# Kernel optimization log

Hardware: AMD Instinct MI355X
Metric: run time of the kernel (lower is better)

Reference implementation:

```python
import jax, jax.numpy as jnp
import numpy as np

NUM_HEADS = 8
NUM_GROUPS = 8
EPS = 1e-5


def group_norm(x, gamma, beta):
    # x: [B, C, H, W], 8 groups over channel dim
    B, C, H, W = x.shape
    xg = x.reshape(B, NUM_GROUPS, C // NUM_GROUPS, H, W)
    mean = xg.mean(axis=(2, 3, 4), keepdims=True)
    var = xg.var(axis=(2, 3, 4), keepdims=True)
    xn = ((xg - mean) * jax.lax.rsqrt(var + EPS)).reshape(B, C, H, W)
    return xn * gamma[None, :, None, None] + beta[None, :, None, None]


def conv1x1(x, w, b):
    # w: [O, C] (1x1 conv kernel squeezed), x: [B, C, H, W]
    return jnp.einsum('oc,bchw->bohw', w, x) + b[None, :, None, None]


def setup_inputs() -> dict:
    key = jax.random.key(0)
    ks = jax.random.split(key, 6)
    B, C, H, W = 16, 512, 32, 32
    x = jax.random.normal(ks[0], (B, C, H, W), dtype=jnp.float32)
    norm_w = jnp.ones((C,), jnp.float32)
    norm_b = jnp.zeros((C,), jnp.float32)
    s = 1.0 / np.sqrt(C)
    qkv_w = jax.random.uniform(ks[1], (3 * C, C), jnp.float32, -s, s)
    qkv_b = jax.random.uniform(ks[2], (3 * C,), jnp.float32, -s, s)
    proj_w = jax.random.uniform(ks[3], (C, C), jnp.float32, -s, s)
    proj_b = jax.random.uniform(ks[4], (C,), jnp.float32, -s, s)
    return {"x": x, "norm_w": norm_w, "norm_b": norm_b,
            "qkv_w": qkv_w, "qkv_b": qkv_b, "proj_w": proj_w, "proj_b": proj_b}


def reference(x, norm_w, norm_b, qkv_w, qkv_b, proj_w, proj_b):
    B, C, H, W = x.shape
    hd = C // NUM_HEADS  # head dim
    h = group_norm(x, norm_w, norm_b)
    qkv = conv1x1(h, qkv_w, qkv_b)                 # [B, 3C, H, W]
    q, k, v = jnp.split(qkv, 3, axis=1)
    q = q.reshape(B, NUM_HEADS, hd, H * W)
    k = k.reshape(B, NUM_HEADS, hd, H * W)
    v = v.reshape(B, NUM_HEADS, hd, H * W)
    scale = hd ** (-0.5)
    attn = jax.nn.softmax(jnp.einsum('bhci,bhcj->bhij', q, k) * scale, axis=-1)
    h = jnp.einsum('bhij,bhcj->bhci', attn, v).reshape(B, C, H, W)
    h = conv1x1(h, proj_w, proj_b)
    return x + h
```

## Files before the change

kernel.cpp:

```cpp
#include <hip/hip_runtime.h>
#include <hip/hip_bf16.h>


typedef __bf16 bf16;
typedef __attribute__((ext_vector_type(8))) __bf16 bf16x8;
typedef __attribute__((ext_vector_type(4))) float f32x4;
typedef __attribute__((ext_vector_type(16))) float f32x16;
typedef __attribute__((ext_vector_type(4))) unsigned int u32x4;

#define SCALE_Q 0.18033688f

__device__ __forceinline__ bf16x8 ld8(const bf16* p) {
    return *reinterpret_cast<const bf16x8*>(p);
}

__device__ __forceinline__ void gl_lds16(const void* g, void* l) {
    __builtin_amdgcn_global_load_lds(
        (const __attribute__((address_space(1))) void*)g,
        (__attribute__((address_space(3))) void*)l, 16, 0, 0);
}

__global__ __launch_bounds__(256) void cvt_fp32_bf16(const float* __restrict__ src,
                                                     bf16* __restrict__ dst, int n) {
    int i = (blockIdx.x * blockDim.x + threadIdx.x) * 4;
    int stride = gridDim.x * blockDim.x * 4;
    for (; i < n; i += stride) {
        float4 f = *reinterpret_cast<const float4*>(src + i);
        dst[i + 0] = (bf16)f.x;
        dst[i + 1] = (bf16)f.y;
        dst[i + 2] = (bf16)f.z;
        dst[i + 3] = (bf16)f.w;
    }
}

__global__ __launch_bounds__(256) void gn_stats(const float* __restrict__ x,
                                                float2* __restrict__ stats) {
    int bg = blockIdx.x;
    const float* base = x + (size_t)bg * 65536;
    float s = 0.f, sq = 0.f;
    for (int i = threadIdx.x * 4; i < 65536; i += 256 * 4) {
        float4 f = *reinterpret_cast<const float4*>(base + i);
        s += f.x + f.y + f.z + f.w;
        sq += f.x * f.x + f.y * f.y + f.z * f.z + f.w * f.w;
    }
    #pragma unroll
    for (int off = 32; off > 0; off >>= 1) {
        s += __shfl_down(s, off);
        sq += __shfl_down(sq, off);
    }
    __shared__ float ls[4], lq[4];
    int wave = threadIdx.x >> 6, lane = threadIdx.x & 63;
    if (lane == 0) { ls[wave] = s; lq[wave] = sq; }
    __syncthreads();
    if (threadIdx.x == 0) {
        s = ls[0] + ls[1] + ls[2] + ls[3];
        sq = lq[0] + lq[1] + lq[2] + lq[3];
        float mean = s * (1.f / 65536.f);
        float var = sq * (1.f / 65536.f) - mean * mean;
        stats[bg] = make_float2(mean, rsqrtf(var + 1e-5f));
    }
}

__global__ __launch_bounds__(256) void gn_apply_t(const float* __restrict__ x,
                                                  const float* __restrict__ gamma,
                                                  const float* __restrict__ beta,
                                                  const float2* __restrict__ stats,
                                                  bf16* __restrict__ hnT) {
    int b = blockIdx.z, ct = blockIdx.y, pt = blockIdx.x;
    __shared__ float tile[64][65];
    int t = threadIdx.x;
    const float* xb = x + ((size_t)b * 512 + ct * 64) * 1024 + pt * 64;
    #pragma unroll
    for (int r = 0; r < 16; r++) {
        int cl = r * 4 + (t >> 6);
        int pl = t & 63;
        tile[cl][pl] = xb[(size_t)cl * 1024 + pl];
    }
    __syncthreads();
    float2 mr = stats[b * 8 + ct];
    int cl = t & 63;
    float g = gamma[ct * 64 + cl], be = beta[ct * 64 + cl];
    bf16* ob = hnT + ((size_t)b * 1024 + pt * 64) * 512 + ct * 64;
    #pragma unroll
    for (int r = 0; r < 16; r++) {
        int pl = r * 4 + (t >> 6);
        float v = (tile[cl][pl] - mr.x) * mr.y * g + be;
        ob[(size_t)pl * 512 + cl] = (bf16)v;
    }
}

__device__ __forceinline__ void gemm_stage(const bf16* __restrict__ A,
                                           const bf16* __restrict__ B,
                                           char* smem, int buf,
                                           int m_blk, int n_blk, int k0,
                                           int wave, int lane) {
    char* Al = smem + buf * 32768;
    char* Bl = Al + 16384;
    #pragma unroll
    for (int i = 0; i < 4; i++) {
        int seg = i * 4 + wave;
        int r = seg * 8 + (lane >> 3);
        int cg = (lane & 7) ^ (r & 7);
        gl_lds16((const char*)(A + (size_t)(m_blk + r) * 512 + k0) + cg * 16,
                 Al + seg * 1024);
        gl_lds16((const char*)(B + (size_t)(n_blk + r) * 512 + k0) + cg * 16,
                 Bl + seg * 1024);
    }
}

__device__ __forceinline__ void gemm_compute(const char* smem, int buf,
                                             int wave, int lane,
                                             f32x4 (&acc)[4][4]) {
    const char* Al = smem + buf * 32768;
    const char* Bl = Al + 16384;
    int l15 = lane & 15, hi = lane >> 4;
    int mb = (wave >> 1) * 64, nb = (wave & 1) * 64;
    #pragma unroll
    for (int kc = 0; kc < 2; kc++) {
        int ck = kc * 4 + hi;
        bf16x8 a[4], b[4];
        #pragma unroll
        for (int mf = 0; mf < 4; mf++) {
            int row = mb + mf * 16 + l15;
            a[mf] = *reinterpret_cast<const bf16x8*>(Al + row * 128 + (ck ^ (row & 7)) * 16);
        }
        #pragma unroll
        for (int nf = 0; nf < 4; nf++) {
            int row = nb + nf * 16 + l15;
            b[nf] = *reinterpret_cast<const bf16x8*>(Bl + row * 128 + (ck ^ (row & 7)) * 16);
        }
        #pragma unroll
        for (int mf = 0; mf < 4; mf++)
            #pragma unroll
            for (int nf = 0; nf < 4; nf++)
                acc[mf][nf] = __builtin_amdgcn_mfma_f32_16x16x32_bf16(
                    a[mf], b[nf], acc[mf][nf], 0, 0, 0);
    }
}

#define GEMM_LDS_LOOP(A_, B_)                                   \
    __shared__ char smem[65536];                                \
    f32x4 acc[4][4] = {};                                       \
    {                                                           \
        gemm_stage(A_, B_, smem, 0, m_blk, n_blk, 0, wave, lane); \
        __syncthreads();                                        \
        int buf = 0;                                            \
        for (int ks = 0; ks < 8; ks++) {                        \
            if (ks < 7)                                         \
                gemm_stage(A_, B_, smem, buf ^ 1, m_blk, n_blk, (ks + 1) * 64, wave, lane); \
            gemm_compute(smem, buf, wave, lane, acc);           \
            __syncthreads();                                    \
            buf ^= 1;                                           \
        }                                                       \
    }

__global__ __launch_bounds__(256, 2) void gemm_qk(const bf16* __restrict__ hnT,
                                                  const bf16* __restrict__ wqkv,
                                                  const float* __restrict__ qkv_b,
                                                  bf16* __restrict__ qk_t) {
    int b = blockIdx.z;
    int wave = threadIdx.x >> 6, lane = threadIdx.x & 63;
    int m_blk = blockIdx.x * 128;
    int n_blk = blockIdx.y * 128;
    const bf16* A = hnT + (size_t)b * 1024 * 512;
    GEMM_LDS_LOOP(A, wqkv)
    bf16* out = qk_t + (size_t)b * 1024 * 1024;
    int l15 = lane & 15;
    int col0 = n_blk + (wave & 1) * 64 + l15;
    int row0 = m_blk + (wave >> 1) * 64 + (lane >> 4) * 4;
    #pragma unroll
    for (int nf = 0; nf < 4; nf++) {
        int col = col0 + nf * 16;
        float bias = qkv_b[col];
        float scl = (col < 512) ? SCALE_Q : 1.0f;
        #pragma unroll
        for (int mf = 0; mf < 4; mf++)
            #pragma unroll
            for (int r = 0; r < 4; r++)
                out[(size_t)(row0 + mf * 16 + r) * 1024 + col] =
                    (bf16)((acc[mf][nf][r] + bias) * scl);
    }
}

__global__ __launch_bounds__(256, 2) void gemm_v(const bf16* __restrict__ wv,
                                                 const bf16* __restrict__ hnT,
                                                 const float* __restrict__ qkv_b,
                                                 bf16* __restrict__ vbuf) {
    int b = blockIdx.z;
    int wave = threadIdx.x >> 6, lane = threadIdx.x & 63;
    int m_blk = blockIdx.x * 128;
    int n_blk = blockIdx.y * 128;
    const bf16* Bm = hnT + (size_t)b * 1024 * 512;
    GEMM_LDS_LOOP(wv, Bm)
    bf16* out = vbuf + (size_t)b * 512 * 1024;
    int l15 = lane & 15;
    int col0 = n_blk + (wave & 1) * 64 + l15;
    int row0 = m_blk + (wave >> 1) * 64 + (lane >> 4) * 4;
    #pragma unroll
    for (int mf = 0; mf < 4; mf++)
        #pragma unroll
        for (int r = 0; r < 4; r++) {
            int row = row0 + mf * 16 + r;
            float bias = qkv_b[1024 + row];
            #pragma unroll
            for (int nf = 0; nf < 4; nf++)
                out[(size_t)row * 1024 + col0 + nf * 16] = (bf16)(acc[mf][nf][r] + bias);
        }
}

__global__ __launch_bounds__(256, 2) void gemm_proj(const bf16* __restrict__ wproj,
                                                    const bf16* __restrict__ attnT,
                                                    const float* __restrict__ proj_b,
                                                    const float* __restrict__ x,
                                                    float* __restrict__ out) {
    int b = blockIdx.z;
    int wave = threadIdx.x >> 6, lane = threadIdx.x & 63;
    int m_blk = blockIdx.x * 128;
    int n_blk = blockIdx.y * 128;
    const bf16* Bm = attnT + (size_t)b * 1024 * 512;
    GEMM_LDS_LOOP(wproj, Bm)
    const float* xb = x + (size_t)b * 512 * 1024;
    float* ob = out + (size_t)b * 512 * 1024;
    int l15 = lane & 15;
    int col0 = n_blk + (wave & 1) * 64 + l15;
    int row0 = m_blk + (wave >> 1) * 64 + (lane >> 4) * 4;
    #pragma unroll
    for (int mf = 0; mf < 4; mf++)
        #pragma unroll
        for (int r = 0; r < 4; r++) {
            int row = row0 + mf * 16 + r;
            float bias = proj_b[row];
            #pragma unroll
            for (int nf = 0; nf < 4; nf++) {
                size_t idx = (size_t)row * 1024 + col0 + nf * 16;
                ob[idx] = acc[mf][nf][r] + bias + xb[idx];
            }
        }
}

__global__ __launch_bounds__(256, 4) void attn_kernel(const bf16* __restrict__ qk_t,
                                                      const bf16* __restrict__ vbuf,
                                                      bf16* __restrict__ attnT) {
    int flat = blockIdx.x;
    int it = flat >> 7;
    int bh = flat & 127;
    int b = bh >> 3, h = bh & 7;
    int wave = threadIdx.x >> 6, lane = threadIdx.x & 63;
    int l31 = lane & 31, hi = lane >> 5;
    int i0 = it * 128 + wave * 32;
    const bf16* qkb = qk_t + (size_t)b * 1024 * 1024;
    const bf16* kbase = qkb + 512 + h * 64;
    const bf16* vb = vbuf + ((size_t)b * 512 + h * 64) * 1024;

    __shared__ __align__(16) char smem[32768];

    bf16x8 bq[4];
    #pragma unroll
    for (int kc = 0; kc < 4; kc++)
        bq[kc] = ld8(qkb + (size_t)(i0 + l31) * 1024 + h * 64 + kc * 16 + hi * 8);

    f32x16 oacc[2] = {};
    float l_part = 0.f;

#define ATTN_STAGE(bufi, j0_)                                                        \
    {                                                                                \
        char* Kl = smem + (bufi) * 16384;                                            \
        char* Vl = Kl + 8192;                                                        \
        _Pragma("unroll")                                                            \
        for (int i = 0; i < 2; i++) {                                                \
            int seg = wave + i * 4;                                                  \
            int r = seg * 8 + (lane >> 3);                                           \
            int cg = (lane & 7) ^ (r & 7);                                           \
            gl_lds16((const char*)(kbase + (size_t)((j0_) + r) * 1024) + cg * 16,    \
                     Kl + seg * 1024);                                               \
            gl_lds16((const char*)(vb + (size_t)r * 1024 + (j0_)) + cg * 16,         \
                     Vl + seg * 1024);                                               \
        }                                                                            \
    }

    ATTN_STAGE(0, 0)
    __syncthreads();
    int buf = 0;

    for (int t = 0; t < 16; t++) {
        if (t < 15) ATTN_STAGE(buf ^ 1, (t + 1) * 64)

        const char* Kl = smem + buf * 16384;
        const char* Vl = Kl + 8192;
        int rx = l31 & 7;

        bf16x8 kf[2][4];
        #pragma unroll
        for (int jb = 0; jb < 2; jb++)
            #pragma unroll
            for (int kc = 0; kc < 4; kc++)
                kf[jb][kc] = *reinterpret_cast<const bf16x8*>(
                    Kl + (jb * 32 + l31) * 128 + (((kc & 1) * 2 + hi + (kc >> 1) * 4) ^ rx) * 16);

        f32x16 s[2] = {};
        #pragma unroll
        for (int kc = 0; kc < 4; kc++) {
            s[0] = __builtin_amdgcn_mfma_f32_32x32x16_bf16(kf[0][kc], bq[kc], s[0], 0, 0, 0);
            s[1] = __builtin_amdgcn_mfma_f32_32x32x16_bf16(kf[1][kc], bq[kc], s[1], 0, 0, 0);
        }

        bf16x8 vf[2][4];
        #pragma unroll
        for (int df = 0; df < 2; df++)
            #pragma unroll
            for (int ks = 0; ks < 4; ks++)
                vf[df][ks] = *reinterpret_cast<const bf16x8*>(
                    Vl + (df * 32 + l31) * 128 + ((ks * 2 + hi) ^ rx) * 16);

        unsigned int pk0[2][4], pk1[2][4];
        #pragma unroll
        for (int jb = 0; jb < 2; jb++)
            #pragma unroll
            for (int m = 0; m < 4; m++) {
                float e0 = exp2f(s[jb][m * 4 + 0]);
                float e1 = exp2f(s[jb][m * 4 + 1]);
                float e2 = exp2f(s[jb][m * 4 + 2]);
                float e3 = exp2f(s[jb][m * 4 + 3]);
                l_part += (e0 + e1) + (e2 + e3);
                asm("v_cvt_pk_bf16_f32 %0, %1, %2" : "=v"(pk0[jb][m]) : "v"(e0), "v"(e1));
                asm("v_cvt_pk_bf16_f32 %0, %1, %2" : "=v"(pk1[jb][m]) : "v"(e2), "v"(e3));
            }

        bf16x8 af[4];
        #pragma unroll
        for (int jb = 0; jb < 2; jb++)
            #pragma unroll
            for (int tt = 0; tt < 2; tt++) {
                unsigned int a0 = pk0[jb][tt * 2], b0 = pk0[jb][tt * 2 + 1];
                unsigned int a1 = pk1[jb][tt * 2], b1 = pk1[jb][tt * 2 + 1];
                asm("v_permlane32_swap_b32 %0, %1" : "+v"(a0), "+v"(b0));
                asm("v_permlane32_swap_b32 %0, %1" : "+v"(a1), "+v"(b1));
                u32x4 w = {a0, a1, b0, b1};
                af[jb * 2 + tt] = __builtin_bit_cast(bf16x8, w);
            }

        #pragma unroll
        for (int ks = 0; ks < 4; ks++) {
            oacc[0] = __builtin_amdgcn_mfma_f32_32x32x16_bf16(af[ks], vf[0][ks], oacc[0], 0, 0, 0);
            oacc[1] = __builtin_amdgcn_mfma_f32_32x32x16_bf16(af[ks], vf[1][ks], oacc[1], 0, 0, 0);
        }

        __syncthreads();
        buf ^= 1;
    }
#undef ATTN_STAGE

    float lsum = l_part + __shfl_xor(l_part, 32);
    float inv = 1.f / lsum;

    bf16* O_l = (bf16*)smem;
    #pragma unroll
    for (int reg = 0; reg < 16; reg++) {
        int qrow = (reg & 3) + 8 * (reg >> 2) + 4 * hi;
        float iv = __shfl(inv, qrow);
        O_l[(wave * 32 + qrow) * 72 + l31]      = (bf16)(oacc[0][reg] * iv);
        O_l[(wave * 32 + qrow) * 72 + 32 + l31] = (bf16)(oacc[1][reg] * iv);
    }
    __syncthreads();
    {
        int tt = threadIdx.x;
        int il = tt >> 1, half = tt & 1;
        const bf16* lsrc = O_l + il * 72 + half * 32;
        bf16* gdst = attnT + ((size_t)b * 1024 + it * 128 + il) * 512 + h * 64 + half * 32;
        #pragma unroll
        for (int k = 0; k < 4; k++)
            *reinterpret_cast<bf16x8*>(gdst + k * 8) =
                *reinterpret_cast<const bf16x8*>(lsrc + k * 8);
    }
}

extern "C" void kernel_launch(void* const* d_in, const int* in_sizes, int n_in,
                              void* d_out, int out_size, void* d_ws, size_t ws_size,
                              hipStream_t stream) {
    (void)in_sizes; (void)n_in; (void)out_size; (void)ws_size;
    const float* x      = (const float*)d_in[0];
    const float* norm_w = (const float*)d_in[1];
    const float* norm_b = (const float*)d_in[2];
    const float* qkv_w  = (const float*)d_in[3];
    const float* qkv_b  = (const float*)d_in[4];
    const float* proj_w = (const float*)d_in[5];
    const float* proj_b = (const float*)d_in[6];
    float* out = (float*)d_out;

    char* w = (char*)d_ws;
    bf16* wqkv  = (bf16*)w;
    bf16* wproj = wqkv + (size_t)1536 * 512;
    float2* stats = (float2*)(wproj + (size_t)512 * 512);
    bf16* hnT   = (bf16*)((char*)stats + 1024);
    bf16* qk_t  = hnT + (size_t)16 * 1024 * 512;
    bf16* vbuf  = qk_t + (size_t)16 * 1024 * 1024;
    bf16* attnT = vbuf + (size_t)16 * 512 * 1024;

    cvt_fp32_bf16<<<768, 256, 0, stream>>>(qkv_w, wqkv, 1536 * 512);
    cvt_fp32_bf16<<<256, 256, 0, stream>>>(proj_w, wproj, 512 * 512);
    gn_stats<<<128, 256, 0, stream>>>(x, stats);
    gn_apply_t<<<dim3(16, 8, 16), 256, 0, stream>>>(x, norm_w, norm_b, stats, hnT);
    gemm_qk<<<dim3(8, 8, 16), 256, 0, stream>>>(hnT, wqkv, qkv_b, qk_t);
    gemm_v<<<dim3(4, 8, 16), 256, 0, stream>>>(wqkv + (size_t)1024 * 512, hnT, qkv_b, vbuf);
    attn_kernel<<<1024, 256, 0, stream>>>(qk_t, vbuf, attnT);
    gemm_proj<<<dim3(4, 8, 16), 256, 0, stream>>>(wproj, attnT, proj_b, x, out);
}
```

Measured before the change: 147.8 us.

## Fuse weight casts, groupnorm passes and QKV GEMMs; relax attention pipeline barriers

Merges the two weight-conversion kernels into one launch. Fuses the groupnorm stats and apply-transpose into one kernel with one block per (batch, group). Merges the Q/K and V GEMMs into a single launch split by blockIdx.y. The attention loop now uses raw s_barrier with explicit vmcnt waits instead of __syncthreads, so the next tile's loads can overlap compute, and the K-fragment LDS index pattern is changed. Fewer launches and less sync are the goal; the risks are that 128 groupnorm blocks underuse the GPU and that the new K indexing may not match the Q fragment order.

```diff
diff --git a/kernel.cpp b/kernel.cpp
--- a/kernel.cpp
+++ b/kernel.cpp
@@ -20,25 +20,31 @@
         (__attribute__((address_space(3))) void*)l, 16, 0, 0);
 }
 
-__global__ __launch_bounds__(256) void cvt_fp32_bf16(const float* __restrict__ src,
-                                                     bf16* __restrict__ dst, int n) {
-    int i = (blockIdx.x * blockDim.x + threadIdx.x) * 4;
-    int stride = gridDim.x * blockDim.x * 4;
-    for (; i < n; i += stride) {
-        float4 f = *reinterpret_cast<const float4*>(src + i);
-        dst[i + 0] = (bf16)f.x;
-        dst[i + 1] = (bf16)f.y;
-        dst[i + 2] = (bf16)f.z;
-        dst[i + 3] = (bf16)f.w;
-    }
-}
-
-__global__ __launch_bounds__(256) void gn_stats(const float* __restrict__ x,
-                                                float2* __restrict__ stats) {
+__global__ __launch_bounds__(256) void cvt_weights(const float* __restrict__ qkv_w,
+                                                   const float* __restrict__ proj_w,
+                                                   bf16* __restrict__ dst) {
+    const int N1 = 1536 * 512;
+    int i = (blockIdx.x * 256 + threadIdx.x) * 4;
+    float4 f = (i < N1) ? *reinterpret_cast<const float4*>(qkv_w + i)
+                        : *reinterpret_cast<const float4*>(proj_w + (i - N1));
+    dst[i + 0] = (bf16)f.x;
+    dst[i + 1] = (bf16)f.y;
+    dst[i + 2] = (bf16)f.z;
+    dst[i + 3] = (bf16)f.w;
+}
+
+__global__ __launch_bounds__(256) void gn_fused(const float* __restrict__ x,
+                                                const float* __restrict__ gamma,
+                                                const float* __restrict__ beta,
+                                                bf16* __restrict__ hnT) {
     int bg = blockIdx.x;
+    int b = bg >> 3, g = bg & 7;
     const float* base = x + (size_t)bg * 65536;
+    int t = threadIdx.x;
+    int wave = t >> 6, lane = t & 63;
+
     float s = 0.f, sq = 0.f;
-    for (int i = threadIdx.x * 4; i < 65536; i += 256 * 4) {
+    for (int i = t * 4; i < 65536; i += 256 * 4) {
         float4 f = *reinterpret_cast<const float4*>(base + i);
         s += f.x + f.y + f.z + f.w;
         sq += f.x * f.x + f.y * f.y + f.z * f.z + f.w * f.w;
@@ -49,43 +55,38 @@
         sq += __shfl_down(sq, off);
     }
     __shared__ float ls[4], lq[4];
-    int wave = threadIdx.x >> 6, lane = threadIdx.x & 63;
+    __shared__ float2 st;
     if (lane == 0) { ls[wave] = s; lq[wave] = sq; }
     __syncthreads();
-    if (threadIdx.x == 0) {
+    if (t == 0) {
         s = ls[0] + ls[1] + ls[2] + ls[3];
         sq = lq[0] + lq[1] + lq[2] + lq[3];
         float mean = s * (1.f / 65536.f);
         float var = sq * (1.f / 65536.f) - mean * mean;
-        stats[bg] = make_float2(mean, rsqrtf(var + 1e-5f));
-    }
-}
-
-__global__ __launch_bounds__(256) void gn_apply_t(const float* __restrict__ x,
-                                                  const float* __restrict__ gamma,
-                                                  const float* __restrict__ beta,
-                                                  const float2* __restrict__ stats,
-                                                  bf16* __restrict__ hnT) {
-    int b = blockIdx.z, ct = blockIdx.y, pt = blockIdx.x;
+        st = make_float2(mean, rsqrtf(var + 1e-5f));
+    }
+    __syncthreads();
+    float mean = st.x, rstd = st.y;
+
     __shared__ float tile[64][65];
-    int t = threadIdx.x;
-    const float* xb = x + ((size_t)b * 512 + ct * 64) * 1024 + pt * 64;
-    #pragma unroll
-    for (int r = 0; r < 16; r++) {
-        int cl = r * 4 + (t >> 6);
-        int pl = t & 63;
-        tile[cl][pl] = xb[(size_t)cl * 1024 + pl];
-    }
-    __syncthreads();
-    float2 mr = stats[b * 8 + ct];
     int cl = t & 63;
-    float g = gamma[ct * 64 + cl], be = beta[ct * 64 + cl];
-    bf16* ob = hnT + ((size_t)b * 1024 + pt * 64) * 512 + ct * 64;
-    #pragma unroll
-    for (int r = 0; r < 16; r++) {
-        int pl = r * 4 + (t >> 6);
-        float v = (tile[cl][pl] - mr.x) * mr.y * g + be;
-        ob[(size_t)pl * 512 + cl] = (bf16)v;
+    float ga = gamma[g * 64 + cl] * rstd;
+    float be = beta[g * 64 + cl] - mean * ga;
+    for (int pt = 0; pt < 16; pt++) {
+        const float* xb = base + pt * 64;
+        #pragma unroll
+        for (int r = 0; r < 16; r++) {
+            int crow = r * 4 + (t >> 6);
+            tile[crow][t & 63] = xb[(size_t)crow * 1024 + (t & 63)];
+        }
+        __syncthreads();
+        bf16* ob = hnT + ((size_t)b * 1024 + pt * 64) * 512 + g * 64 + cl;
+        #pragma unroll
+        for (int r = 0; r < 16; r++) {
+            int pl = r * 4 + (t >> 6);
+            ob[(size_t)pl * 512] = (bf16)(tile[cl][pl] * ga + be);
+        }
+        __syncthreads();
     }
 }
 
@@ -138,74 +139,71 @@
     }
 }
 
-#define GEMM_LDS_LOOP(A_, B_)                                   \
-    __shared__ char smem[65536];                                \
+#define GEMM_LDS_LOOP(A_, B_, SMEM_)                            \
     f32x4 acc[4][4] = {};                                       \
     {                                                           \
-        gemm_stage(A_, B_, smem, 0, m_blk, n_blk, 0, wave, lane); \
+        gemm_stage(A_, B_, SMEM_, 0, m_blk, n_blk, 0, wave, lane); \
         __syncthreads();                                        \
         int buf = 0;                                            \
         for (int ks = 0; ks < 8; ks++) {                        \
             if (ks < 7)                                         \
-                gemm_stage(A_, B_, smem, buf ^ 1, m_blk, n_blk, (ks + 1) * 64, wave, lane); \
-            gemm_compute(smem, buf, wave, lane, acc);           \
+                gemm_stage(A_, B_, SMEM_, buf ^ 1, m_blk, n_blk, (ks + 1) * 64, wave, lane); \
+            gemm_compute(SMEM_, buf, wave, lane, acc);          \
             __syncthreads();                                    \
             buf ^= 1;                                           \
         }                                                       \
     }
 
-__global__ __launch_bounds__(256, 2) void gemm_qk(const bf16* __restrict__ hnT,
-                                                  const bf16* __restrict__ wqkv,
-                                                  const float* __restrict__ qkv_b,
-                                                  bf16* __restrict__ qk_t) {
+__global__ __launch_bounds__(256, 2) void gemm_qkv(const bf16* __restrict__ hnT,
+                                                   const bf16* __restrict__ wqkv,
+                                                   const float* __restrict__ qkv_b,
+                                                   bf16* __restrict__ qk_t,
+                                                   bf16* __restrict__ vbuf) {
+    __shared__ char smem[65536];
     int b = blockIdx.z;
     int wave = threadIdx.x >> 6, lane = threadIdx.x & 63;
-    int m_blk = blockIdx.x * 128;
-    int n_blk = blockIdx.y * 128;
-    const bf16* A = hnT + (size_t)b * 1024 * 512;
-    GEMM_LDS_LOOP(A, wqkv)
-    bf16* out = qk_t + (size_t)b * 1024 * 1024;
     int l15 = lane & 15;
-    int col0 = n_blk + (wave & 1) * 64 + l15;
-    int row0 = m_blk + (wave >> 1) * 64 + (lane >> 4) * 4;
-    #pragma unroll
-    for (int nf = 0; nf < 4; nf++) {
-        int col = col0 + nf * 16;
-        float bias = qkv_b[col];
-        float scl = (col < 512) ? SCALE_Q : 1.0f;
+    int y = blockIdx.y;
+    if (y < 8) {
+        int m_blk = blockIdx.x * 128;
+        int n_blk = y * 128;
+        const bf16* A = hnT + (size_t)b * 1024 * 512;
+        GEMM_LDS_LOOP(A, wqkv, smem)
+        bf16* out = qk_t + (size_t)b * 1024 * 1024;
+        int col0 = n_blk + (wave & 1) * 64 + l15;
+        int row0 = m_blk + (wave >> 1) * 64 + (lane >> 4) * 4;
+        #pragma unroll
+        for (int nf = 0; nf < 4; nf++) {
+            int col = col0 + nf * 16;
+            float bias = qkv_b[col];
+            float scl = (col < 512) ? SCALE_Q : 1.0f;
+            #pragma unroll
+            for (int mf = 0; mf < 4; mf++)
+                #pragma unroll
+                for (int r = 0; r < 4; r++)
+                    out[(size_t)(row0 + mf * 16 + r) * 1024 + col] =
+                        (bf16)((acc[mf][nf][r] + bias) * scl);
+        }
+    } else {
+        int m_blk = (y - 8) * 128;
+        int n_blk = blockIdx.x * 128;
+        const bf16* A = wqkv + (size_t)1024 * 512;
+        const bf16* Bm = hnT + (size_t)b * 1024 * 512;
+        GEMM_LDS_LOOP(A, Bm, smem)
+        bf16* out = vbuf + (size_t)b * 512 * 1024;
+        int col0 = n_blk + (wave & 1) * 64 + l15;
+        int row0 = m_blk + (wave >> 1) * 64 + (lane >> 4) * 4;
         #pragma unroll
         for (int mf = 0; mf < 4; mf++)
             #pragma unroll
-            for (int r = 0; r < 4; r++)
-                out[(size_t)(row0 + mf * 16 + r) * 1024 + col] =
-                    (bf16)((acc[mf][nf][r] + bias) * scl);
-    }
-}
-
-__global__ __launch_bounds__(256, 2) void gemm_v(const bf16* __restrict__ wv,
-                                                 const bf16* __restrict__ hnT,
-                                                 const float* __restrict__ qkv_b,
-                                                 bf16* __restrict__ vbuf) {
-    int b = blockIdx.z;
-    int wave = threadIdx.x >> 6, lane = threadIdx.x & 63;
-    int m_blk = blockIdx.x * 128;
-    int n_blk = blockIdx.y * 128;
-    const bf16* Bm = hnT + (size_t)b * 1024 * 512;
-    GEMM_LDS_LOOP(wv, Bm)
-    bf16* out = vbuf + (size_t)b * 512 * 1024;
-    int l15 = lane & 15;
-    int col0 = n_blk + (wave & 1) * 64 + l15;
-    int row0 = m_blk + (wave >> 1) * 64 + (lane >> 4) * 4;
-    #pragma unroll
-    for (int mf = 0; mf < 4; mf++)
-        #pragma unroll
-        for (int r = 0; r < 4; r++) {
-            int row = row0 + mf * 16 + r;
-            float bias = qkv_b[1024 + row];
-            #pragma unroll
-            for (int nf = 0; nf < 4; nf++)
-                out[(size_t)row * 1024 + col0 + nf * 16] = (bf16)(acc[mf][nf][r] + bias);
-        }
+            for (int r = 0; r < 4; r++) {
+                int row = row0 + mf * 16 + r;
+                float bias = qkv_b[1024 + row];
+                #pragma unroll
+                for (int nf = 0; nf < 4; nf++)
+                    out[(size_t)row * 1024 + col0 + nf * 16] = (bf16)(acc[mf][nf][r] + bias);
+            }
+    }
 }
 
 __global__ __launch_bounds__(256, 2) void gemm_proj(const bf16* __restrict__ wproj,
@@ -213,12 +211,13 @@
                                                     const float* __restrict__ proj_b,
                                                     const float* __restrict__ x,
                                                     float* __restrict__ out) {
+    __shared__ char smem[65536];
     int b = blockIdx.z;
     int wave = threadIdx.x >> 6, lane = threadIdx.x & 63;
     int m_blk = blockIdx.x * 128;
     int n_blk = blockIdx.y * 128;
     const bf16* Bm = attnT + (size_t)b * 1024 * 512;
-    GEMM_LDS_LOOP(wproj, Bm)
+    GEMM_LDS_LOOP(wproj, Bm, smem)
     const float* xb = x + (size_t)b * 512 * 1024;
     float* ob = out + (size_t)b * 512 * 1024;
     int l15 = lane & 15;
@@ -279,11 +278,19 @@
     }
 
     ATTN_STAGE(0, 0)
-    __syncthreads();
     int buf = 0;
 
     for (int t = 0; t < 16; t++) {
-        if (t < 15) ATTN_STAGE(buf ^ 1, (t + 1) * 64)
+        asm volatile("" ::: "memory");
+        __builtin_amdgcn_s_barrier();
+        if (t < 15) {
+            ATTN_STAGE(buf ^ 1, (t + 1) * 64)
+            asm volatile("s_waitcnt vmcnt(4)" ::: "memory");
+        } else {
+            asm volatile("s_waitcnt vmcnt(0)" ::: "memory");
+        }
+        __builtin_amdgcn_s_barrier();
+        asm volatile("" ::: "memory");
 
         const char* Kl = smem + buf * 16384;
         const char* Vl = Kl + 8192;
@@ -295,7 +302,7 @@
             #pragma unroll
             for (int kc = 0; kc < 4; kc++)
                 kf[jb][kc] = *reinterpret_cast<const bf16x8*>(
-                    Kl + (jb * 32 + l31) * 128 + (((kc & 1) * 2 + hi + (kc >> 1) * 4) ^ rx) * 16);
+                    Kl + (jb * 32 + l31) * 128 + ((kc * 2 + hi) ^ rx) * 16);
 
         f32x16 s[2] = {};
         #pragma unroll
@@ -345,13 +352,14 @@
             oacc[1] = __builtin_amdgcn_mfma_f32_32x32x16_bf16(af[ks], vf[1][ks], oacc[1], 0, 0, 0);
         }
 
-        __syncthreads();
         buf ^= 1;
     }
 #undef ATTN_STAGE
 
     float lsum = l_part + __shfl_xor(l_part, 32);
     float inv = 1.f / lsum;
+
+    __syncthreads();
 
     bf16* O_l = (bf16*)smem;
     #pragma unroll
@@ -390,18 +398,14 @@
     char* w = (char*)d_ws;
     bf16* wqkv  = (bf16*)w;
     bf16* wproj = wqkv + (size_t)1536 * 512;
-    float2* stats = (float2*)(wproj + (size_t)512 * 512);
-    bf16* hnT   = (bf16*)((char*)stats + 1024);
+    bf16* hnT   = wproj + (size_t)512 * 512;
     bf16* qk_t  = hnT + (size_t)16 * 1024 * 512;
     bf16* vbuf  = qk_t + (size_t)16 * 1024 * 1024;
     bf16* attnT = vbuf + (size_t)16 * 512 * 1024;
 
-    cvt_fp32_bf16<<<768, 256, 0, stream>>>(qkv_w, wqkv, 1536 * 512);
-    cvt_fp32_bf16<<<256, 256, 0, stream>>>(proj_w, wproj, 512 * 512);
-    gn_stats<<<128, 256, 0, stream>>>(x, stats);
-    gn_apply_t<<<dim3(16, 8, 16), 256, 0, stream>>>(x, norm_w, norm_b, stats, hnT);
-    gemm_qk<<<dim3(8, 8, 16), 256, 0, stream>>>(hnT, wqkv, qkv_b, qk_t);
-    gemm_v<<<dim3(4, 8, 16), 256, 0, stream>>>(wqkv + (size_t)1024 * 512, hnT, qkv_b, vbuf);
+    cvt_weights<<<1024, 256, 0, stream>>>(qkv_w, proj_w, wqkv);
+    gn_fused<<<128, 256, 0, stream>>>(x, norm_w, norm_b, hnT);
+    gemm_qkv<<<dim3(8, 12, 16), 256, 0, stream>>>(hnT, wqkv, qkv_b, qk_t, vbuf);
     attn_kernel<<<1024, 256, 0, stream>>>(qk_t, vbuf, attnT);
     gemm_proj<<<dim3(4, 8, 16), 256, 0, stream>>>(wproj, attnT, proj_b, x, out);
 }
```

Measured after the change: 147.6 us. About the same (-0.2%).
